# Performance work log

Hardware: AMD Instinct MI355X
Metric: run time of the kernel (lower is better)

## Reference

```python
import jax, jax.numpy as jnp
import numpy as np

B, TE, TD, HE, HD = 8, 256, 256, 512, 512


def setup_inputs() -> dict:
    key = jax.random.key(0)
    k1, k2, k3, k4, k5 = jax.random.split(key, 5)
    return {
        "encoder_out_seq": jax.random.normal(k1, (B, TE, HE), dtype=jnp.float32),
        "decoder_out_seq": jax.random.normal(k2, (B, TD, HD), dtype=jnp.float32),
        "W_a": jax.random.normal(k3, (HE, HE), dtype=jnp.float32) * 0.05,
        "U_a": jax.random.normal(k4, (HD, HE), dtype=jnp.float32) * 0.05,
        "V_a": jax.random.normal(k5, (HE, 1), dtype=jnp.float32) * 0.05,
    }


def reference(encoder_out_seq, decoder_out_seq, W_a, U_a, V_a):
    # Bahdanau additive attention, vectorized over all decoder timesteps.
    # Hoist encoder projection (the K.rnn version recomputed this each step).
    Ws = jnp.einsum('bth,hk->btk', encoder_out_seq, W_a)      # [B, Te, He]
    Uh = jnp.einsum('bdh,hk->bdk', decoder_out_seq, U_a)     # [B, Td, He]
    # tanh(S.Wa + hj.Ua) -> score via V_a, softmax over encoder axis Te
    scores = jnp.einsum('bdtk,k->bdt',
                        jnp.tanh(Ws[:, None, :, :] + Uh[:, :, None, :]),
                        V_a[:, 0])                            # [B, Td, Te]
    e = jax.nn.softmax(scores, axis=-1)                       # energies
    c = jnp.einsum('bdt,bth->bdh', e, encoder_out_seq)        # contexts [B, Td, He]
    return c, e
```

## Files before the change

### kernel.cpp

```cpp
#include <hip/hip_runtime.h>


#define BB  8
#define TEE 256
#define TDD 256
#define HH  512
#define C2LOG2E 2.8853900817779268f
#define SLAB ((size_t)BB * TDD * TEE)

typedef __attribute__((ext_vector_type(8))) short  short8;
typedef __attribute__((ext_vector_type(4))) float  floatx4;

__device__ __forceinline__ unsigned short f2bf(float f) {
  unsigned int u = __builtin_bit_cast(unsigned int, f);
  u += 0x7FFFu + ((u >> 16) & 1u);
  return (unsigned short)(u >> 16);
}

__global__ __launch_bounds__(256) void prep_kernel(
    const float* __restrict__ Wa, const float* __restrict__ Ua,
    const float* __restrict__ enc,
    unsigned short* __restrict__ WTa, unsigned short* __restrict__ WTu,
    unsigned short* __restrict__ encT)
{
  __shared__ float tile[64][65];
  const int c = threadIdx.x & 63, r4 = threadIdx.x >> 6;
  const int z = blockIdx.z;

  if (z < 2) {
    const float* W = z ? Ua : Wa;
    unsigned short* WT = z ? WTu : WTa;
    const int k0 = blockIdx.x * 64, n0 = blockIdx.y * 64;
    #pragma unroll
    for (int i = 0; i < 16; ++i) {
      int kr = i * 4 + r4;
      tile[kr][c] = W[(size_t)(k0 + kr) * HH + n0 + c];
    }
    __syncthreads();
    #pragma unroll
    for (int i = 0; i < 16; ++i) {
      int nr = i * 4 + r4;
      WT[(size_t)(n0 + nr) * HH + k0 + c] = f2bf(tile[c][nr] * C2LOG2E);
    }
  } else {
    if (blockIdx.y >= 4) return;
    const int b = z - 2;
    const int h0 = blockIdx.x * 64, t0 = blockIdx.y * 64;
    #pragma unroll
    for (int i = 0; i < 16; ++i) {
      int tr = i * 4 + r4;
      tile[tr][c] = enc[((size_t)b * TEE + t0 + tr) * HH + h0 + c];
    }
    __syncthreads();
    #pragma unroll
    for (int i = 0; i < 16; ++i) {
      int hr = i * 4 + r4;
      encT[((size_t)b * HH + h0 + hr) * TEE + t0 + c] = f2bf(tile[c][hr]);
    }
  }
}

__global__ __launch_bounds__(256) void proj_exp(
    const float* __restrict__ enc, const float* __restrict__ dec,
    const unsigned short* __restrict__ WTa, const unsigned short* __restrict__ WTu,
    float* __restrict__ EW, float* __restrict__ EU)
{
  const float* X = blockIdx.z ? dec : enc;
  const unsigned short* WT = blockIdx.z ? WTu : WTa;
  float* Y = blockIdx.z ? EU : EW;
  const int lane = threadIdx.x & 63, w = threadIdx.x >> 6;
  const int m0 = blockIdx.x * 64 + w * 16, n0 = blockIdx.y * 64;
  const int r15 = lane & 15, g = lane >> 4;

  floatx4 acc[4] = {{0.f,0.f,0.f,0.f},{0.f,0.f,0.f,0.f},
                    {0.f,0.f,0.f,0.f},{0.f,0.f,0.f,0.f}};
  const float* ap = X + (size_t)(m0 + r15) * HH + g * 8;
  const unsigned short* bp0 = WT + (size_t)(n0 + r15) * HH + g * 8;

  for (int k0 = 0; k0 < HH; k0 += 32) {
    float4 a0 = *(const float4*)(ap + k0);
    float4 a1 = *(const float4*)(ap + k0 + 4);
    short8 a;
    a[0]=(short)f2bf(a0.x); a[1]=(short)f2bf(a0.y);
    a[2]=(short)f2bf(a0.z); a[3]=(short)f2bf(a0.w);
    a[4]=(short)f2bf(a1.x); a[5]=(short)f2bf(a1.y);
    a[6]=(short)f2bf(a1.z); a[7]=(short)f2bf(a1.w);
    #pragma unroll
    for (int nt = 0; nt < 4; ++nt) {
      short8 bv = *(const short8*)(bp0 + (size_t)nt * 16 * HH + k0);
      acc[nt] = __builtin_amdgcn_mfma_f32_16x16x32_bf16(a, bv, acc[nt], 0, 0, 0);
    }
  }
  #pragma unroll
  for (int nt = 0; nt < 4; ++nt) {
    float* yp = Y + (size_t)(m0 + g * 4) * HH + n0 + nt * 16 + r15;
    #pragma unroll
    for (int r = 0; r < 4; ++r) {
      float v = fminf(fmaxf(acc[nt][r], -126.f), 126.f);
      yp[(size_t)r * HH] = __builtin_amdgcn_exp2f(v);
    }
  }
}

__global__ __launch_bounds__(256) void score_rt(
    const float* __restrict__ EW, const float* __restrict__ EU,
    const float* __restrict__ Va, float* __restrict__ Apart)
{
  __shared__ float swT[2][32][68];
  __shared__ float suT[2][32][68];

  const int b  = blockIdx.z;
  const int ks = blockIdx.x >> 2;
  const int t0 = (blockIdx.x & 3) * 64;
  const int d0 = blockIdx.y * 64;
  const int kbase = ks * 128;
  const int tid = threadIdx.x;
  const int tx = tid & 15, ty = tid >> 4;
  const int sr = tid >> 2, fq = tid & 3;
  const int kq = fq * 4;

  const float* wsrc = EW + ((size_t)(b * TEE) + t0 + sr) * HH + kbase + kq;
  const float* usrc = EU + ((size_t)(b * TDD) + d0 + sr) * HH + kbase + kq;

  float acc[4][4] = {};

#define STAGE(BUF_, W0_, W1_, U0_, U1_) {                         \
    swT[BUF_][kq + 0][sr] = W0_.x; swT[BUF_][kq + 1][sr] = W0_.y; \
    swT[BUF_][kq + 2][sr] = W0_.z; swT[BUF_][kq + 3][sr] = W0_.w; \
    swT[BUF_][kq +16][sr] = W1_.x; swT[BUF_][kq +17][sr] = W1_.y; \
    swT[BUF_][kq +18][sr] = W1_.z; swT[BUF_][kq +19][sr] = W1_.w; \
    suT[BUF_][kq + 0][sr] = U0_.x; suT[BUF_][kq + 1][sr] = U0_.y; \
    suT[BUF_][kq + 2][sr] = U0_.z; suT[BUF_][kq + 3][sr] = U0_.w; \
    suT[BUF_][kq +16][sr] = U1_.x; suT[BUF_][kq +17][sr] = U1_.y; \
    suT[BUF_][kq +18][sr] = U1_.z; suT[BUF_][kq +19][sr] = U1_.w; }

  {
    float4 w0 = *(const float4*)(wsrc);
    float4 w1 = *(const float4*)(wsrc + 16);
    float4 u0 = *(const float4*)(usrc);
    float4 u1 = *(const float4*)(usrc + 16);
    STAGE(0, w0, w1, u0, u1)
  }

  for (int ch = 0; ch < 4; ++ch) {
    float4 nw0, nw1, nu0, nu1;
    const bool more = (ch + 1) < 4;
    if (more) {
      const int kc = (ch + 1) * 32;
      nw0 = *(const float4*)(wsrc + kc);
      nw1 = *(const float4*)(wsrc + kc + 16);
      nu0 = *(const float4*)(usrc + kc);
      nu1 = *(const float4*)(usrc + kc + 16);
    }
    __syncthreads();

    const int cb = ch & 1;
    const float* vb = Va + kbase + ch * 32;
#define T1(WI_, UJ_, AJI_) { \
    float z_ = fmaf((WI_), (UJ_), 1.0f); \
    AJI_ = fmaf(v, __builtin_amdgcn_rcpf(z_), AJI_); }

    #pragma unroll 4
    for (int k = 0; k < 32; ++k) {
      floatx4 w = *(const floatx4*)&swT[cb][k][tx * 4];
      floatx4 u = *(const floatx4*)&suT[cb][k][ty * 4];
      float v = vb[k];
      #pragma unroll
      for (int j = 0; j < 4; ++j) {
        float uj = u[j];
        T1(w[0], uj, acc[j][0]) T1(w[1], uj, acc[j][1])
        T1(w[2], uj, acc[j][2]) T1(w[3], uj, acc[j][3])
      }
    }
#undef T1

    if (more) STAGE((ch + 1) & 1, nw0, nw1, nu0, nu1)
  }
#undef STAGE

  float* Ap = Apart + (size_t)ks * SLAB;
  #pragma unroll
  for (int j = 0; j < 4; ++j) {
    const int d = d0 + ty * 4 + j;
    floatx4 o = {acc[j][0], acc[j][1], acc[j][2], acc[j][3]};
    *(floatx4*)(Ap + ((size_t)(b * TDD) + d) * TEE + t0 + tx * 4) = o;
  }
}

__global__ __launch_bounds__(256) void ctx_fused(
    const float* __restrict__ Apart, const unsigned short* __restrict__ encT,
    float* __restrict__ c, float* __restrict__ e_out)
{
  __shared__ unsigned short pe[16][264];

  const int b  = blockIdx.z;
  const int d0 = blockIdx.x * 16;
  const int h0 = blockIdx.y * 256;
  const int lane = threadIdx.x & 63, w = threadIdx.x >> 6;

  {
    const int row  = w * 4 + (lane >> 4);
    const int col0 = (lane & 15) * 16;
    const size_t base = ((size_t)(b * TDD) + d0 + row) * TEE + col0;
    float x[16];
    #pragma unroll
    for (int q = 0; q < 4; ++q) {
      floatx4 v = *(const floatx4*)(Apart + base + q * 4);
      x[4*q] = v[0]; x[4*q+1] = v[1]; x[4*q+2] = v[2]; x[4*q+3] = v[3];
    }
    #pragma unroll
    for (int s = 1; s < 4; ++s) {
      #pragma unroll
      for (int q = 0; q < 4; ++q) {
        floatx4 v = *(const floatx4*)(Apart + (size_t)s * SLAB + base + q * 4);
        x[4*q] += v[0]; x[4*q+1] += v[1]; x[4*q+2] += v[2]; x[4*q+3] += v[3];
      }
    }
    float m = x[0];
    #pragma unroll
    for (int j = 1; j < 16; ++j) m = fminf(m, x[j]);
    #pragma unroll
    for (int off = 8; off; off >>= 1) m = fminf(m, __shfl_xor(m, off));
    float p[16], s = 0.f;
    #pragma unroll
    for (int j = 0; j < 16; ++j) {
      p[j] = __builtin_amdgcn_exp2f(C2LOG2E * (m - x[j]));
      s += p[j];
    }
    #pragma unroll
    for (int off = 8; off; off >>= 1) s += __shfl_xor(s, off);
    float r = __builtin_amdgcn_rcpf(s);

    #pragma unroll
    for (int j = 0; j < 16; j += 2) {
      float v0 = p[j] * r, v1 = p[j+1] * r;
      *(ushort2*)&pe[row][col0 + j] = make_ushort2(f2bf(v0), f2bf(v1));
    }
    if (blockIdx.y == 0) {
      float* er = e_out + ((size_t)(b * TDD) + d0 + row) * TEE + col0;
      #pragma unroll
      for (int j = 0; j < 16; ++j) er[j] = p[j] * r;
    }
  }
  __syncthreads();

  const int r15 = lane & 15, g = lane >> 4;
  const int hw = h0 + w * 64;
  floatx4 acc[4] = {{0.f,0.f,0.f,0.f},{0.f,0.f,0.f,0.f},
                    {0.f,0.f,0.f,0.f},{0.f,0.f,0.f,0.f}};
  const unsigned short* bp0 = encT + ((size_t)b * HH + hw + r15) * TEE + g * 8;

  for (int k0 = 0; k0 < TEE; k0 += 32) {
    short8 a = *(const short8*)(&pe[r15][k0 + g * 8]);
    #pragma unroll
    for (int nt = 0; nt < 4; ++nt) {
      short8 bv = *(const short8*)(bp0 + (size_t)nt * 16 * TEE + k0);
      acc[nt] = __builtin_amdgcn_mfma_f32_16x16x32_bf16(a, bv, acc[nt], 0, 0, 0);
    }
  }
  #pragma unroll
  for (int nt = 0; nt < 4; ++nt) {
    float* cp = c + ((size_t)(b * TDD) + d0 + g * 4) * HH + hw + nt * 16 + r15;
    #pragma unroll
    for (int r = 0; r < 4; ++r) cp[(size_t)r * HH] = acc[nt][r];
  }
}

extern "C" void kernel_launch(void* const* d_in, const int* in_sizes, int n_in,
                              void* d_out, int out_size, void* d_ws, size_t ws_size,
                              hipStream_t stream) {
  const float* enc = (const float*)d_in[0];
  const float* dec = (const float*)d_in[1];
  const float* Wa  = (const float*)d_in[2];
  const float* Ua  = (const float*)d_in[3];
  const float* Va  = (const float*)d_in[4];

  float* c_out = (float*)d_out;
  float* e_out = c_out + (size_t)BB * TDD * HH;

  unsigned short* WTa  = (unsigned short*)d_ws;
  unsigned short* WTu  = WTa + (size_t)HH * HH;
  unsigned short* encT = WTu + (size_t)HH * HH;
  float* EW    = (float*)(encT + (size_t)BB * HH * TEE);
  float* EU    = EW + (size_t)BB * TEE * HH;
  float* Apart = EU + (size_t)BB * TDD * HH;

  prep_kernel<<<dim3(8, 8, 10),  256, 0, stream>>>(Wa, Ua, enc, WTa, WTu, encT);
  proj_exp   <<<dim3(32, 8, 2),  256, 0, stream>>>(enc, dec, WTa, WTu, EW, EU);
  score_rt   <<<dim3(16, 4, 8),  256, 0, stream>>>(EW, EU, Va, Apart);
  ctx_fused  <<<dim3(16, 2, 8),  256, 0, stream>>>(Apart, encT, c_out, e_out);
}
```

Before: 75.15 us.

## Split score K-dimension into eight slices, widen ctx grid, prefetch proj operands

The score kernel now splits the hidden dimension into 8 partial slices of 64 instead of 4 of 128. This doubles the grid to 1024 blocks for better occupancy across CUs. The context kernel halves its per-block H tile to double its block count, and its softmax now sums 8 partial slabs, which costs extra reads of the partial-score buffer. The projection kernel adds register double-buffering of the next K-step's A and B operands, to hide global load latency behind the MFMAs.

```diff
diff --git a/kernel.cpp b/kernel.cpp
--- a/kernel.cpp
+++ b/kernel.cpp
@@ -7,6 +7,7 @@
 #define HH  512
 #define C2LOG2E 2.8853900817779268f
 #define SLAB ((size_t)BB * TDD * TEE)
+#define NKS 8
 
 typedef __attribute__((ext_vector_type(8))) short  short8;
 typedef __attribute__((ext_vector_type(4))) float  floatx4;
@@ -72,31 +73,46 @@
   const int m0 = blockIdx.x * 64 + w * 16, n0 = blockIdx.y * 64;
   const int r15 = lane & 15, g = lane >> 4;
 
-  floatx4 acc[4] = {{0.f,0.f,0.f,0.f},{0.f,0.f,0.f,0.f},
-                    {0.f,0.f,0.f,0.f},{0.f,0.f,0.f,0.f}};
+  floatx4 acc0 = {0.f,0.f,0.f,0.f}, acc1 = {0.f,0.f,0.f,0.f};
+  floatx4 acc2 = {0.f,0.f,0.f,0.f}, acc3 = {0.f,0.f,0.f,0.f};
   const float* ap = X + (size_t)(m0 + r15) * HH + g * 8;
   const unsigned short* bp0 = WT + (size_t)(n0 + r15) * HH + g * 8;
 
+  float4 ca0 = *(const float4*)(ap);
+  float4 ca1 = *(const float4*)(ap + 4);
+  short8 cb0 = *(const short8*)(bp0);
+  short8 cb1 = *(const short8*)(bp0 + (size_t)16 * HH);
+  short8 cb2 = *(const short8*)(bp0 + (size_t)32 * HH);
+  short8 cb3 = *(const short8*)(bp0 + (size_t)48 * HH);
+
   for (int k0 = 0; k0 < HH; k0 += 32) {
-    float4 a0 = *(const float4*)(ap + k0);
-    float4 a1 = *(const float4*)(ap + k0 + 4);
+    float4 na0, na1; short8 nb0, nb1, nb2, nb3;
+    if (k0 + 32 < HH) {
+      na0 = *(const float4*)(ap + k0 + 32);
+      na1 = *(const float4*)(ap + k0 + 36);
+      nb0 = *(const short8*)(bp0 + k0 + 32);
+      nb1 = *(const short8*)(bp0 + (size_t)16 * HH + k0 + 32);
+      nb2 = *(const short8*)(bp0 + (size_t)32 * HH + k0 + 32);
+      nb3 = *(const short8*)(bp0 + (size_t)48 * HH + k0 + 32);
+    }
     short8 a;
-    a[0]=(short)f2bf(a0.x); a[1]=(short)f2bf(a0.y);
-    a[2]=(short)f2bf(a0.z); a[3]=(short)f2bf(a0.w);
-    a[4]=(short)f2bf(a1.x); a[5]=(short)f2bf(a1.y);
-    a[6]=(short)f2bf(a1.z); a[7]=(short)f2bf(a1.w);
-    #pragma unroll
-    for (int nt = 0; nt < 4; ++nt) {
-      short8 bv = *(const short8*)(bp0 + (size_t)nt * 16 * HH + k0);
-      acc[nt] = __builtin_amdgcn_mfma_f32_16x16x32_bf16(a, bv, acc[nt], 0, 0, 0);
-    }
-  }
+    a[0]=(short)f2bf(ca0.x); a[1]=(short)f2bf(ca0.y);
+    a[2]=(short)f2bf(ca0.z); a[3]=(short)f2bf(ca0.w);
+    a[4]=(short)f2bf(ca1.x); a[5]=(short)f2bf(ca1.y);
+    a[6]=(short)f2bf(ca1.z); a[7]=(short)f2bf(ca1.w);
+    acc0 = __builtin_amdgcn_mfma_f32_16x16x32_bf16(a, cb0, acc0, 0, 0, 0);
+    acc1 = __builtin_amdgcn_mfma_f32_16x16x32_bf16(a, cb1, acc1, 0, 0, 0);
+    acc2 = __builtin_amdgcn_mfma_f32_16x16x32_bf16(a, cb2, acc2, 0, 0, 0);
+    acc3 = __builtin_amdgcn_mfma_f32_16x16x32_bf16(a, cb3, acc3, 0, 0, 0);
+    ca0 = na0; ca1 = na1; cb0 = nb0; cb1 = nb1; cb2 = nb2; cb3 = nb3;
+  }
+  floatx4 aall[4] = {acc0, acc1, acc2, acc3};
   #pragma unroll
   for (int nt = 0; nt < 4; ++nt) {
     float* yp = Y + (size_t)(m0 + g * 4) * HH + n0 + nt * 16 + r15;
     #pragma unroll
     for (int r = 0; r < 4; ++r) {
-      float v = fminf(fmaxf(acc[nt][r], -126.f), 126.f);
+      float v = fminf(fmaxf(aall[nt][r], -126.f), 126.f);
       yp[(size_t)r * HH] = __builtin_amdgcn_exp2f(v);
     }
   }
@@ -113,7 +129,7 @@
   const int ks = blockIdx.x >> 2;
   const int t0 = (blockIdx.x & 3) * 64;
   const int d0 = blockIdx.y * 64;
-  const int kbase = ks * 128;
+  const int kbase = ks * 64;
   const int tid = threadIdx.x;
   const int tx = tid & 15, ty = tid >> 4;
   const int sr = tid >> 2, fq = tid & 3;
@@ -142,19 +158,17 @@
     STAGE(0, w0, w1, u0, u1)
   }
 
-  for (int ch = 0; ch < 4; ++ch) {
+  for (int ch = 0; ch < 2; ++ch) {
     float4 nw0, nw1, nu0, nu1;
-    const bool more = (ch + 1) < 4;
+    const bool more = (ch == 0);
     if (more) {
-      const int kc = (ch + 1) * 32;
-      nw0 = *(const float4*)(wsrc + kc);
-      nw1 = *(const float4*)(wsrc + kc + 16);
-      nu0 = *(const float4*)(usrc + kc);
-      nu1 = *(const float4*)(usrc + kc + 16);
+      nw0 = *(const float4*)(wsrc + 32);
+      nw1 = *(const float4*)(wsrc + 48);
+      nu0 = *(const float4*)(usrc + 32);
+      nu1 = *(const float4*)(usrc + 48);
     }
     __syncthreads();
 
-    const int cb = ch & 1;
     const float* vb = Va + kbase + ch * 32;
 #define T1(WI_, UJ_, AJI_) { \
     float z_ = fmaf((WI_), (UJ_), 1.0f); \
@@ -162,8 +176,8 @@
 
     #pragma unroll 4
     for (int k = 0; k < 32; ++k) {
-      floatx4 w = *(const floatx4*)&swT[cb][k][tx * 4];
-      floatx4 u = *(const floatx4*)&suT[cb][k][ty * 4];
+      floatx4 w = *(const floatx4*)&swT[ch][k][tx * 4];
+      floatx4 u = *(const floatx4*)&suT[ch][k][ty * 4];
       float v = vb[k];
       #pragma unroll
       for (int j = 0; j < 4; ++j) {
@@ -174,7 +188,7 @@
     }
 #undef T1
 
-    if (more) STAGE((ch + 1) & 1, nw0, nw1, nu0, nu1)
+    if (more) STAGE(1, nw0, nw1, nu0, nu1)
   }
 #undef STAGE
 
@@ -195,7 +209,7 @@
 
   const int b  = blockIdx.z;
   const int d0 = blockIdx.x * 16;
-  const int h0 = blockIdx.y * 256;
+  const int h0 = blockIdx.y * 128;
   const int lane = threadIdx.x & 63, w = threadIdx.x >> 6;
 
   {
@@ -209,7 +223,7 @@
       x[4*q] = v[0]; x[4*q+1] = v[1]; x[4*q+2] = v[2]; x[4*q+3] = v[3];
     }
     #pragma unroll
-    for (int s = 1; s < 4; ++s) {
+    for (int s = 1; s < NKS; ++s) {
       #pragma unroll
       for (int q = 0; q < 4; ++q) {
         floatx4 v = *(const floatx4*)(Apart + (size_t)s * SLAB + base + q * 4);
@@ -245,24 +259,23 @@
   __syncthreads();
 
   const int r15 = lane & 15, g = lane >> 4;
-  const int hw = h0 + w * 64;
-  floatx4 acc[4] = {{0.f,0.f,0.f,0.f},{0.f,0.f,0.f,0.f},
-                    {0.f,0.f,0.f,0.f},{0.f,0.f,0.f,0.f}};
+  const int hw = h0 + w * 32;
+  floatx4 acc0 = {0.f,0.f,0.f,0.f}, acc1 = {0.f,0.f,0.f,0.f};
   const unsigned short* bp0 = encT + ((size_t)b * HH + hw + r15) * TEE + g * 8;
 
   for (int k0 = 0; k0 < TEE; k0 += 32) {
     short8 a = *(const short8*)(&pe[r15][k0 + g * 8]);
-    #pragma unroll
-    for (int nt = 0; nt < 4; ++nt) {
-      short8 bv = *(const short8*)(bp0 + (size_t)nt * 16 * TEE + k0);
-      acc[nt] = __builtin_amdgcn_mfma_f32_16x16x32_bf16(a, bv, acc[nt], 0, 0, 0);
-    }
-  }
+    short8 bv0 = *(const short8*)(bp0 + k0);
+    short8 bv1 = *(const short8*)(bp0 + (size_t)16 * TEE + k0);
+    acc0 = __builtin_amdgcn_mfma_f32_16x16x32_bf16(a, bv0, acc0, 0, 0, 0);
+    acc1 = __builtin_amdgcn_mfma_f32_16x16x32_bf16(a, bv1, acc1, 0, 0, 0);
+  }
+  floatx4 aall[2] = {acc0, acc1};
   #pragma unroll
-  for (int nt = 0; nt < 4; ++nt) {
+  for (int nt = 0; nt < 2; ++nt) {
     float* cp = c + ((size_t)(b * TDD) + d0 + g * 4) * HH + hw + nt * 16 + r15;
     #pragma unroll
-    for (int r = 0; r < 4; ++r) cp[(size_t)r * HH] = acc[nt][r];
+    for (int r = 0; r < 4; ++r) cp[(size_t)r * HH] = aall[nt][r];
   }
 }
 
@@ -287,6 +300,6 @@
 
   prep_kernel<<<dim3(8, 8, 10),  256, 0, stream>>>(Wa, Ua, enc, WTa, WTu, encT);
   proj_exp   <<<dim3(32, 8, 2),  256, 0, stream>>>(enc, dec, WTa, WTu, EW, EU);
-  score_rt   <<<dim3(16, 4, 8),  256, 0, stream>>>(EW, EU, Va, Apart);
-  ctx_fused  <<<dim3(16, 2, 8),  256, 0, stream>>>(Apart, encT, c_out, e_out);
-}
+  score_rt   <<<dim3(32, 4, 8),  256, 0, stream>>>(EW, EU, Va, Apart);
+  ctx_fused  <<<dim3(16, 4, 8),  256, 0, stream>>>(Apart, encT, c_out, e_out);
+}
```

After: 76.84 us. 2.2% more time.
